# Kernel optimization log

Hardware: AMD Instinct MI355X
Metric: run time of the kernel (lower is better)

## Reference

```python
import jax, jax.numpy as jnp
import numpy as np

DIM, NH, HD = 1536, 12, 128
C = HD // 2            # 64 complex (half) dims per head
BANDS = (C - 2 * (C // 3), C // 3, C // 3)   # (22, 21, 21) for T/H/W
EPS = 1e-6
F, Hg, Wg = 6, 20, 32
S = F * Hg * Wg
MAX_LEN = 1024


def _rope_tables(max_len=MAX_LEN):
    # Wan-style 1D rope params per band, concatenated along channel dim -> [max_len, 64]
    pos = np.arange(max_len, dtype=np.float64)
    cos_l, sin_l = [], []
    for bd in BANDS:
        inv = 1.0 / (10000.0 ** (np.arange(bd, dtype=np.float64) / bd))
        ang = np.outer(pos, inv)
        cos_l.append(np.cos(ang))
        sin_l.append(np.sin(ang))
    return (np.concatenate(cos_l, 1).astype(np.float32),
            np.concatenate(sin_l, 1).astype(np.float32))


def setup_inputs() -> dict:
    key = jax.random.key(0)
    ks = jax.random.split(key, 8)
    std = 0.02
    fc, fs = _rope_tables()
    return {
        "x": jax.random.normal(ks[0], (1, S, DIM), jnp.float32),
        "Wq": jax.random.normal(ks[1], (DIM, DIM), jnp.float32) * std,
        "bq": jnp.zeros((DIM,), jnp.float32),
        "Wk": jax.random.normal(ks[2], (DIM, DIM), jnp.float32) * std,
        "bk": jnp.zeros((DIM,), jnp.float32),
        "Wv": jax.random.normal(ks[3], (DIM, DIM), jnp.float32) * std,
        "bv": jnp.zeros((DIM,), jnp.float32),
        "Wo": jax.random.normal(ks[4], (DIM, DIM), jnp.float32) * std,
        "bo": jnp.zeros((DIM,), jnp.float32),
        "gq": jnp.ones((DIM,), jnp.float32),
        "gk": jnp.ones((DIM,), jnp.float32),
        "freqs_cos": jnp.asarray(fc),
        "freqs_sin": jnp.asarray(fs),
        "f": F, "h": Hg, "w": Wg,
    }


def _rmsnorm(t, g):
    t = t.astype(jnp.float32)
    return t * jax.lax.rsqrt(jnp.mean(t * t, axis=-1, keepdims=True) + EPS) * g


def _grid_freqs(tab, f, h, w):
    # tab: [max_len, 64] -> [f*h*w, 64] via T/H/W band broadcast (mirrors torch expand+cat)
    o1, o2 = BANDS[0], BANDS[0] + BANDS[1]
    t = jnp.broadcast_to(tab[:f, None, None, :o1], (f, h, w, BANDS[0]))
    hh = jnp.broadcast_to(tab[None, :h, None, o1:o2], (f, h, w, BANDS[1]))
    ww = jnp.broadcast_to(tab[None, None, :w, o2:C], (f, h, w, BANDS[2]))
    return jnp.concatenate([t, hh, ww], axis=-1).reshape(f * h * w, 1, C)


def _rope_apply(t, fc, fs):
    # t: [B, S, n, d]; complex mul (a+ib)*(cos+isin) on pairs of channels
    B, Sl, n, d = t.shape
    tr = t.astype(jnp.float32).reshape(B, Sl, n, C, 2)
    a, b = tr[..., 0], tr[..., 1]
    fc = fc[None]  # [1, S, 1, C]
    fs = fs[None]
    out_r = a * fc - b * fs
    out_i = a * fs + b * fc
    return jnp.stack([out_r, out_i], axis=-1).reshape(B, Sl, n, d)


def reference(x, Wq, bq, Wk, bk, Wv, bv, Wo, bo, gq, gk, freqs_cos, freqs_sin, f, h, w):
    B, Sl, _ = x.shape
    q = _rmsnorm(x @ Wq.T + bq, gq).reshape(B, Sl, NH, HD)
    k = _rmsnorm(x @ Wk.T + bk, gk).reshape(B, Sl, NH, HD)
    v = (x @ Wv.T + bv).reshape(B, Sl, NH, HD)

    fc = _grid_freqs(freqs_cos, f, h, w)
    fs = _grid_freqs(freqs_sin, f, h, w)
    q = _rope_apply(q, fc, fs)
    k = _rope_apply(k, fc, fs)

    scale = 1.0 / jnp.sqrt(jnp.float32(HD))
    scores = jnp.einsum('bqnd,bknd->bnqk', q, k) * scale
    p = jax.nn.softmax(scores, axis=-1)
    o = jnp.einsum('bnqk,bknd->bqnd', p, v.astype(jnp.float32))
    o = o.reshape(B, Sl, DIM)
    return o @ Wo.T + bo
```

## Files before the change

kernel.cpp:

```cpp
#include <hip/hip_runtime.h>
#include <hip/hip_bf16.h>
#include <cstdint>

#define DIM 1536
#define NHEADS 12
#define HD 128
#define SEQ 3840
#define SCL2F 0.1275365308119098f
#define THRRAW 90.50966799187809f

typedef float f32x4 __attribute__((ext_vector_type(4)));
typedef __bf16 bf16x8 __attribute__((ext_vector_type(8)));
typedef __bf16 bf16x4 __attribute__((ext_vector_type(4)));
typedef __bf16 bf16x2 __attribute__((ext_vector_type(2)));
typedef unsigned int u32;
typedef u32 u32x4 __attribute__((ext_vector_type(4)));

#define GLLD(g, l) __builtin_amdgcn_global_load_lds( \
    (const __attribute__((address_space(1))) void*)(g), \
    (__attribute__((address_space(3))) void*)(l), 16, 0, 0)

__global__ __launch_bounds__(256) void cvt_bf16_5(
    const float* __restrict__ s0, const float* __restrict__ s1, const float* __restrict__ s2,
    const float* __restrict__ s3, const float* __restrict__ s4,
    __bf16* __restrict__ d0, __bf16* __restrict__ d1, __bf16* __restrict__ d2,
    __bf16* __restrict__ d3, __bf16* __restrict__ d4,
    int n4_0, int n4_w) {
    const float* src; __bf16* dst; int n4;
    switch (blockIdx.y) {
        case 0: src = s0; dst = d0; n4 = n4_0; break;
        case 1: src = s1; dst = d1; n4 = n4_w; break;
        case 2: src = s2; dst = d2; n4 = n4_w; break;
        case 3: src = s3; dst = d3; n4 = n4_w; break;
        default: src = s4; dst = d4; n4 = n4_w; break;
    }
    int i = blockIdx.x * 256 + threadIdx.x;
    if (i < n4) {
        f32x4 v = ((const f32x4*)src)[i];
        bf16x4 o;
        o[0] = (__bf16)v[0]; o[1] = (__bf16)v[1];
        o[2] = (__bf16)v[2]; o[3] = (__bf16)v[3];
        ((bf16x4*)dst)[i] = o;
    }
}

template <int OUTF32>
__global__ __launch_bounds__(256, 2) void gemm256(
    const __bf16* __restrict__ A,
    const __bf16* __restrict__ B0, const __bf16* __restrict__ B1, const __bf16* __restrict__ B2,
    const float* __restrict__ bias0, const float* __restrict__ bias1, const float* __restrict__ bias2,
    void* __restrict__ C0v, void* __restrict__ C1v, void* __restrict__ C2v,
    int N, int K) {
    const __bf16* B = B0; const float* bias = bias0; void* Cv = C0v;
    if (blockIdx.z == 1) { B = B1; bias = bias1; Cv = C1v; }
    else if (blockIdx.z == 2) { B = B2; bias = bias2; Cv = C2v; }

    __shared__ __bf16 sA[3][256 * 32];
    __shared__ __bf16 sB[3][128 * 32];

    const int t = threadIdx.x;
    const int wid = t >> 6, lane = t & 63;
    const int lr = lane & 15, lg = lane >> 4;
    const int wr = (wid >> 1) * 128, wc = (wid & 1) * 64;

    const __bf16* pa = A + ((long long)blockIdx.y * 256 + (t >> 2)) * K + (t & 3) * 8;
    const __bf16* pb = B + ((long long)blockIdx.x * 128 + (t >> 2)) * K + (t & 3) * 8;
    const int ldsbase = wid * 512;

    auto stage = [&](int kk, int bufi) {
#pragma unroll
        for (int r = 0; r < 4; r++)
            GLLD(pa + (long long)(r * 64) * K + kk, &sA[bufi][r * 2048 + ldsbase]);
#pragma unroll
        for (int r = 0; r < 2; r++)
            GLLD(pb + (long long)(r * 64) * K + kk, &sB[bufi][r * 2048 + ldsbase]);
    };

    f32x4 acc[8][4] = {};
    const int NT = K / 32;

    stage(0, 0);
    stage(32, 1);
    asm volatile("s_waitcnt vmcnt(6)" ::: "memory");
    __builtin_amdgcn_s_barrier();
    __builtin_amdgcn_sched_barrier(0);

    int c0 = 0, c2 = 2;
#pragma unroll 1
    for (int i = 0; i < NT; i++) {
        const __bf16* sAc = &sA[0][0] + c0 * (256 * 32);
        const __bf16* sBc = &sB[0][0] + c0 * (128 * 32);
        bf16x8 af[8], bfr[4];
#pragma unroll
        for (int mI = 0; mI < 8; mI++)
            af[mI] = *(const bf16x8*)(sAc + (wr + mI * 16 + lr) * 32 + lg * 8);
#pragma unroll
        for (int nI = 0; nI < 4; nI++)
            bfr[nI] = *(const bf16x8*)(sBc + (wc + nI * 16 + lr) * 32 + lg * 8);
        if (i + 2 < NT) stage((i + 2) * 32, c2);

        __builtin_amdgcn_s_setprio(1);
#pragma unroll
        for (int mI = 0; mI < 8; mI++) {
            acc[mI][0] = __builtin_amdgcn_mfma_f32_16x16x32_bf16(af[mI], bfr[0], acc[mI][0], 0, 0, 0);
            acc[mI][1] = __builtin_amdgcn_mfma_f32_16x16x32_bf16(af[mI], bfr[1], acc[mI][1], 0, 0, 0);
        }
        __builtin_amdgcn_s_setprio(0);
        __builtin_amdgcn_s_barrier();
        __builtin_amdgcn_s_setprio(1);
#pragma unroll
        for (int mI = 0; mI < 8; mI++) {
            acc[mI][2] = __builtin_amdgcn_mfma_f32_16x16x32_bf16(af[mI], bfr[2], acc[mI][2], 0, 0, 0);
            acc[mI][3] = __builtin_amdgcn_mfma_f32_16x16x32_bf16(af[mI], bfr[3], acc[mI][3], 0, 0, 0);
        }
        __builtin_amdgcn_s_setprio(0);

        if (i + 2 < NT) asm volatile("s_waitcnt vmcnt(6)" ::: "memory");
        else            asm volatile("s_waitcnt vmcnt(0)" ::: "memory");
        __builtin_amdgcn_s_barrier();
        __builtin_amdgcn_sched_barrier(0);
        c0 = (c0 == 2) ? 0 : c0 + 1;
        c2 = (c2 == 2) ? 0 : c2 + 1;
    }

    const int cb = blockIdx.x * 128 + wc;
    const int rb_ = blockIdx.y * 256 + wr;
#pragma unroll
    for (int nI = 0; nI < 4; nI++) {
        int col = cb + nI * 16 + lr;
        float bv = bias[col];
#pragma unroll
        for (int mI = 0; mI < 8; mI++) {
            int row0 = rb_ + mI * 16 + lg * 4;
#pragma unroll
            for (int r = 0; r < 4; r++) {
                float v = acc[mI][nI][r] + bv;
                if (OUTF32) ((float*)Cv)[(long long)(row0 + r) * N + col] = v;
                else ((__bf16*)Cv)[(long long)(row0 + r) * N + col] = (__bf16)v;
            }
        }
    }
}

__global__ __launch_bounds__(256) void norm_rope2(
    const __bf16* __restrict__ qpre, const __bf16* __restrict__ kpre,
    const float* __restrict__ gq, const float* __restrict__ gk,
    const float* __restrict__ fcos, const float* __restrict__ fsin,
    __bf16* __restrict__ Qb, __bf16* __restrict__ Kb) {
    const __bf16* pre = blockIdx.y ? kpre : qpre;
    const float* gvec = blockIdx.y ? gk : gq;
    __bf16* out = blockIdx.y ? Kb : Qb;
    const int s = blockIdx.x;
    const int t = threadIdx.x;
    float a[3], b[3];
    float ss = 0.f;
#pragma unroll
    for (int j = 0; j < 3; j++) {
        int p = t + 256 * j;
        bf16x2 v = *(const bf16x2*)(pre + (size_t)s * DIM + 2 * p);
        a[j] = (float)v[0]; b[j] = (float)v[1];
        ss += a[j] * a[j] + b[j] * b[j];
    }
    for (int off = 32; off; off >>= 1) ss += __shfl_down(ss, off);
    __shared__ float red[4];
    if ((t & 63) == 0) red[t >> 6] = ss;
    __syncthreads();
    float mean = (red[0] + red[1] + red[2] + red[3]) * (1.f / DIM);
    float rms = rsqrtf(mean + 1e-6f);
    const int fi = s / 640, hi2 = (s % 640) >> 5, wi = s & 31;
#pragma unroll
    for (int j = 0; j < 3; j++) {
        int p = t + 256 * j;
        int c = p & 63;
        int pos = (c < 22) ? fi : ((c < 43) ? hi2 : wi);
        float fc = fcos[pos * 64 + c];
        float fs = fsin[pos * 64 + c];
        float av = a[j] * rms * gvec[2 * p];
        float bv = b[j] * rms * gvec[2 * p + 1];
        float orr = av * fc - bv * fs;
        float oi = av * fs + bv * fc;
        int hh = p >> 6;
        bf16x2 o; o[0] = (__bf16)orr; o[1] = (__bf16)oi;
        *(bf16x2*)(out + ((size_t)hh * SEQ + s) * HD + 2 * c) = o;
    }
}

__global__ __launch_bounds__(256) void transpose_bf16(
    const __bf16* __restrict__ in, __bf16* __restrict__ out) {
    __shared__ __bf16 tile[64][68];
    const int t = threadIdx.x;
    const int sb = blockIdx.x * 64, cb = blockIdx.y * 64;
    const int tx = t & 15, ty = t >> 4;
#pragma unroll
    for (int i = 0; i < 4; i++) {
        int r = ty + i * 16;
        bf16x4 v = *(const bf16x4*)(in + (size_t)(sb + r) * DIM + cb + tx * 4);
        *(bf16x4*)&tile[r][tx * 4] = v;
    }
    __syncthreads();
    int s0 = sb + tx * 4;
    int j = (s0 >> 2) & 7;
    int u = (j < 4) ? (j << 1) : ((j << 1) - 7);
    int sp = (s0 & ~31) + (u << 2);
#pragma unroll
    for (int i = 0; i < 4; i++) {
        int c = ty + i * 16;
        bf16x4 v;
        v[0] = tile[tx * 4 + 0][c]; v[1] = tile[tx * 4 + 1][c];
        v[2] = tile[tx * 4 + 2][c]; v[3] = tile[tx * 4 + 3][c];
        *(bf16x4*)(out + (size_t)(cb + c) * SEQ + sp) = v;
    }
}

__global__ __launch_bounds__(256, 4) void attn(
    const __bf16* __restrict__ Q, const __bf16* __restrict__ Kk,
    const __bf16* __restrict__ Vp, __bf16* __restrict__ O) {
    __shared__ __bf16 Ks[2][32 * 128];
    __shared__ __bf16 Vs[2][128 * 32];
    const int bid = blockIdx.x;
    const int task = (bid & 7) * 90 + (bid >> 3);
    const int h = task / 60;
    const int qb = task % 60;
    const int t = threadIdx.x;
    const int wv = t >> 6;
    const int lane = t & 63;
    const int lq = lane & 15, g = lane >> 4;
    const int q0 = qb * 64 + wv * 16;
    const __bf16* Qh = Q + (size_t)h * SEQ * HD;
    const __bf16* Kh = Kk + (size_t)h * SEQ * HD;
    const __bf16* Vh = Vp + (size_t)h * HD * SEQ;

    bf16x8 qf[4];
#pragma unroll
    for (int c = 0; c < 4; c++)
        qf[c] = *(const bf16x8*)(Qh + (size_t)(q0 + lq) * HD + c * 32 + g * 8);

    f32x4 acc[8] = {};
    float m = -1e30f;
    float lp = 0.f;

    const int krow_in = lane >> 4;
    const int vrow_in = lane >> 2;
    const int vce = (lane & 3) * 8;
    auto stage = [&](int kv0, int b) {
#pragma unroll
        for (int c = wv; c < 16; c += 4) {
            if (c < 8) {
                int r = c * 4 + krow_in;
                int cb = ((lane & 15) * 16) ^ ((r & 7) << 4);
                GLLD(Kh + (size_t)(kv0 + r) * HD + (cb >> 1), &Ks[b][c * 512]);
            } else {
                int cc = c - 8;
                int rd = cc * 16 + vrow_in;
                GLLD(Vh + (size_t)rd * SEQ + kv0 + vce, &Vs[b][cc * 512]);
            }
        }
    };

    stage(0, 0);
    int buf = 0;
    const int kswz = (lq & 7) << 3;
#pragma unroll 1
    for (int i = 0; i < 120; i++) {
        __syncthreads();
        if (i + 1 < 120) stage((i + 1) * 32, buf ^ 1);
        const __bf16* Kb_ = &Ks[buf][0];
        const __bf16* Vb_ = &Vs[buf][0];

        f32x4 sc0 = {0.f, 0.f, 0.f, 0.f}, sc1 = {0.f, 0.f, 0.f, 0.f};
        __builtin_amdgcn_s_setprio(1);
#pragma unroll
        for (int c = 0; c < 4; c++) {
            int cb = (c * 32 + g * 8) ^ kswz;
            bf16x8 k0 = *(const bf16x8*)(Kb_ + lq * 128 + cb);
            bf16x8 k1 = *(const bf16x8*)(Kb_ + (16 + lq) * 128 + cb);
            sc0 = __builtin_amdgcn_mfma_f32_16x16x32_bf16(k0, qf[c], sc0, 0, 0, 0);
            sc1 = __builtin_amdgcn_mfma_f32_16x16x32_bf16(k1, qf[c], sc1, 0, 0, 0);
        }
        __builtin_amdgcn_s_setprio(0);

        bf16x8 vf[8];
#pragma unroll
        for (int dt = 0; dt < 8; dt++)
            vf[dt] = *(const bf16x8*)(Vb_ + (dt * 16 + lq) * 32 + g * 8);

        float pm = fmaxf(fmaxf(fmaxf(sc0[0], sc0[1]), fmaxf(sc0[2], sc0[3])),
                         fmaxf(fmaxf(sc1[0], sc1[1]), fmaxf(sc1[2], sc1[3])));
        if (!__all(pm <= m + THRRAW)) {
            pm = fmaxf(pm, __shfl_xor(pm, 16));
            pm = fmaxf(pm, __shfl_xor(pm, 32));
            float mn = fmaxf(m, pm);
            float al = __builtin_amdgcn_exp2f(SCL2F * (m - mn));
            m = mn; lp *= al;
#pragma unroll
            for (int dt = 0; dt < 8; dt++)
#pragma unroll
                for (int r = 0; r < 4; r++) acc[dt][r] *= al;
        }
        float ms = SCL2F * m;
        float p[8], ls = 0.f;
#pragma unroll
        for (int r = 0; r < 4; r++) { p[r] = __builtin_amdgcn_exp2f(SCL2F * sc0[r] - ms); ls += p[r]; }
#pragma unroll
        for (int r = 0; r < 4; r++) { p[4 + r] = __builtin_amdgcn_exp2f(SCL2F * sc1[r] - ms); ls += p[4 + r]; }
        lp += ls;
        bf16x8 pa;
#pragma unroll
        for (int i2 = 0; i2 < 8; i2++) pa[i2] = (__bf16)p[i2];

        __builtin_amdgcn_s_setprio(1);
#pragma unroll
        for (int dt = 0; dt < 8; dt++)
            acc[dt] = __builtin_amdgcn_mfma_f32_16x16x32_bf16(vf[dt], pa, acc[dt], 0, 0, 0);
        __builtin_amdgcn_s_setprio(0);
        buf ^= 1;
    }

    float lps = lp;
    lps += __shfl_xor(lps, 16);
    lps += __shfl_xor(lps, 32);
    float inv = 1.f / lps;
#pragma unroll
    for (int dt = 0; dt < 8; dt++) {
        bf16x4 o;
#pragma unroll
        for (int r = 0; r < 4; r++) o[r] = (__bf16)(acc[dt][r] * inv);
        *(bf16x4*)(O + (size_t)(q0 + lq) * DIM + h * HD + dt * 16 + g * 4) = o;
    }
}

extern "C" void kernel_launch(void* const* d_in, const int* in_sizes, int n_in,
                              void* d_out, int out_size, void* d_ws, size_t ws_size,
                              hipStream_t stream) {
    const float* x = (const float*)d_in[0];
    const float* Wq = (const float*)d_in[1];
    const float* bq = (const float*)d_in[2];
    const float* Wk = (const float*)d_in[3];
    const float* bk = (const float*)d_in[4];
    const float* Wv = (const float*)d_in[5];
    const float* bv = (const float*)d_in[6];
    const float* Wo = (const float*)d_in[7];
    const float* bo = (const float*)d_in[8];
    const float* gq = (const float*)d_in[9];
    const float* gk = (const float*)d_in[10];
    const float* fcos = (const float*)d_in[11];
    const float* fsin = (const float*)d_in[12];
    float* out = (float*)d_out;

    char* p = (char*)d_ws;
    const size_t SZ_SD = (size_t)SEQ * DIM * 2;
    const size_t SZ_W = (size_t)DIM * DIM * 2;
    __bf16* xb   = (__bf16*)p;  p += SZ_SD;
    __bf16* Wqb  = (__bf16*)p;  p += SZ_W;
    __bf16* Wkb  = (__bf16*)p;  p += SZ_W;
    __bf16* Wvb  = (__bf16*)p;  p += SZ_W;
    __bf16* Wob  = (__bf16*)p;  p += SZ_W;
    __bf16* qpre = (__bf16*)p;  p += SZ_SD;
    __bf16* kpre = (__bf16*)p;  p += SZ_SD;
    __bf16* vpre = (__bf16*)p;  p += SZ_SD;
    __bf16* Kb   = (__bf16*)p;  p += SZ_SD;
    __bf16* Vtb  = (__bf16*)p;  p += SZ_SD;
    __bf16* Qb = xb;
    __bf16* ob = qpre;

    const int n4_x = SEQ * DIM / 4;
    const int n4_w = DIM * DIM / 4;
    cvt_bf16_5<<<dim3((n4_x + 255) / 256, 5), 256, 0, stream>>>(
        x, Wq, Wk, Wv, Wo, xb, Wqb, Wkb, Wvb, Wob, n4_x, n4_w);

    gemm256<0><<<dim3(DIM / 128, SEQ / 256, 3), 256, 0, stream>>>(
        xb, Wqb, Wkb, Wvb, bq, bk, bv, qpre, kpre, vpre, DIM, DIM);

    norm_rope2<<<dim3(SEQ, 2), 256, 0, stream>>>(qpre, kpre, gq, gk, fcos, fsin, Qb, Kb);
    transpose_bf16<<<dim3(SEQ / 64, DIM / 64), 256, 0, stream>>>(vpre, Vtb);

    attn<<<dim3(720), 256, 0, stream>>>(Qb, Kb, Vtb, ob);

    gemm256<1><<<dim3(DIM / 128, SEQ / 256, 1), 256, 0, stream>>>(
        ob, Wob, Wob, Wob, bo, bo, bo, out, out, out, DIM, DIM);
}
```

Baseline: 284.9 us.

## Split attention KV range into two halves with separate merge kernel

Result: slower. 296.0 us (+3.9%).

```diff
diff --git a/kernel.cpp b/kernel.cpp
--- a/kernel.cpp
+++ b/kernel.cpp
@@ -212,7 +212,146 @@
     }
 }
 
-__global__ __launch_bounds__(256, 4) void attn(
+__global__ __launch_bounds__(256, 4) void attn_split(
+    const __bf16* __restrict__ Q, const __bf16* __restrict__ Kk,
+    const __bf16* __restrict__ Vp,
+    float* __restrict__ pacc,
+    float2* __restrict__ pml) {
+    __shared__ __bf16 Ks[2][32 * 128];
+    __shared__ __bf16 Vs[2][128 * 32];
+    const int bid = blockIdx.x;
+    const int task = (bid & 7) * 180 + (bid >> 3);
+    const int half = task & 1;
+    const int hq = task >> 1;
+    const int h = hq / 60;
+    const int qb = hq % 60;
+    const int t = threadIdx.x;
+    const int wv = t >> 6;
+    const int lane = t & 63;
+    const int lq = lane & 15, g = lane >> 4;
+    const int q0 = qb * 64 + wv * 16;
+    const int kvbase = half * (SEQ / 2);
+    const __bf16* Qh = Q + (size_t)h * SEQ * HD;
+    const __bf16* Kh = Kk + (size_t)h * SEQ * HD;
+    const __bf16* Vh = Vp + (size_t)h * HD * SEQ;
+
+    bf16x8 qf[4];
+#pragma unroll
+    for (int c = 0; c < 4; c++)
+        qf[c] = *(const bf16x8*)(Qh + (size_t)(q0 + lq) * HD + c * 32 + g * 8);
+
+    f32x4 acc[8] = {};
+    float m = -1e30f;
+    float lp = 0.f;
+
+    const int krow_in = lane >> 4;
+    const int vrow_in = lane >> 2;
+    const int vce = (lane & 3) * 8;
+    auto stage = [&](int kv0, int b) {
+#pragma unroll
+        for (int c = wv; c < 16; c += 4) {
+            if (c < 8) {
+                int r = c * 4 + krow_in;
+                int cb = ((lane & 15) * 16) ^ ((r & 7) << 4);
+                GLLD(Kh + (size_t)(kv0 + r) * HD + (cb >> 1), &Ks[b][c * 512]);
+            } else {
+                int cc = c - 8;
+                int rd = cc * 16 + vrow_in;
+                GLLD(Vh + (size_t)rd * SEQ + kv0 + vce, &Vs[b][cc * 512]);
+            }
+        }
+    };
+
+    stage(kvbase, 0);
+    int buf = 0;
+    const int kswz = (lq & 7) << 3;
+#pragma unroll 1
+    for (int i = 0; i < 60; i++) {
+        __syncthreads();
+        if (i + 1 < 60) stage(kvbase + (i + 1) * 32, buf ^ 1);
+        const __bf16* Kb_ = &Ks[buf][0];
+        const __bf16* Vb_ = &Vs[buf][0];
+
+        f32x4 sc0 = {0.f, 0.f, 0.f, 0.f}, sc1 = {0.f, 0.f, 0.f, 0.f};
+        __builtin_amdgcn_s_setprio(1);
+#pragma unroll
+        for (int c = 0; c < 4; c++) {
+            int cb = (c * 32 + g * 8) ^ kswz;
+            bf16x8 k0 = *(const bf16x8*)(Kb_ + lq * 128 + cb);
+            bf16x8 k1 = *(const bf16x8*)(Kb_ + (16 + lq) * 128 + cb);
+            sc0 = __builtin_amdgcn_mfma_f32_16x16x32_bf16(k0, qf[c], sc0, 0, 0, 0);
+            sc1 = __builtin_amdgcn_mfma_f32_16x16x32_bf16(k1, qf[c], sc1, 0, 0, 0);
+        }
+        __builtin_amdgcn_s_setprio(0);
+
+        bf16x8 vf[8];
+#pragma unroll
+        for (int dt = 0; dt < 8; dt++)
+            vf[dt] = *(const bf16x8*)(Vb_ + (dt * 16 + lq) * 32 + g * 8);
+
+        float pm = fmaxf(fmaxf(fmaxf(sc0[0], sc0[1]), fmaxf(sc0[2], sc0[3])),
+                         fmaxf(fmaxf(sc1[0], sc1[1]), fmaxf(sc1[2], sc1[3])));
+        if (!__all(pm <= m + THRRAW)) {
+            pm = fmaxf(pm, __shfl_xor(pm, 16));
+            pm = fmaxf(pm, __shfl_xor(pm, 32));
+            float mn = fmaxf(m, pm);
+            float al = __builtin_amdgcn_exp2f(SCL2F * (m - mn));
+            m = mn; lp *= al;
+#pragma unroll
+            for (int dt = 0; dt < 8; dt++)
+#pragma unroll
+                for (int r = 0; r < 4; r++) acc[dt][r] *= al;
+        }
+        float ms = SCL2F * m;
+        float p[8], ls = 0.f;
+#pragma unroll
+        for (int r = 0; r < 4; r++) { p[r] = __builtin_amdgcn_exp2f(SCL2F * sc0[r] - ms); ls += p[r]; }
+#pragma unroll
+        for (int r = 0; r < 4; r++) { p[4 + r] = __builtin_amdgcn_exp2f(SCL2F * sc1[r] - ms); ls += p[4 + r]; }
+        lp += ls;
+        bf16x8 pa;
+#pragma unroll
+        for (int i2 = 0; i2 < 8; i2++) pa[i2] = (__bf16)p[i2];
+
+        __builtin_amdgcn_s_setprio(1);
+#pragma unroll
+        for (int dt = 0; dt < 8; dt++)
+            acc[dt] = __builtin_amdgcn_mfma_f32_16x16x32_bf16(vf[dt], pa, acc[dt], 0, 0, 0);
+        __builtin_amdgcn_s_setprio(0);
+        buf ^= 1;
+    }
+
+    float lps = lp;
+    lps += __shfl_xor(lps, 16);
+    lps += __shfl_xor(lps, 32);
+    const size_t qrow = (size_t)(half * NHEADS + h) * SEQ + q0 + lq;
+    if (g == 0) pml[qrow] = float2{m, lps};
+#pragma unroll
+    for (int dt = 0; dt < 8; dt++)
+        *(f32x4*)(pacc + qrow * HD + dt * 16 + g * 4) = acc[dt];
+}
+
+__global__ __launch_bounds__(256) void attn_merge(
+    const float* __restrict__ pacc, const float2* __restrict__ pml,
+    __bf16* __restrict__ ob) {
+    const int t = threadIdx.x;
+    const int qq = blockIdx.x * 8 + (t >> 5);
+    const int d = (t & 31) * 4;
+    float2 a = pml[qq], b = pml[NHEADS * SEQ + qq];
+    float M = fmaxf(a.x, b.x);
+    float w0 = __builtin_amdgcn_exp2f(SCL2F * (a.x - M));
+    float w1 = __builtin_amdgcn_exp2f(SCL2F * (b.x - M));
+    float den = 1.f / (a.y * w0 + b.y * w1);
+    f32x4 n0 = *(const f32x4*)(pacc + (size_t)qq * HD + d);
+    f32x4 n1 = *(const f32x4*)(pacc + ((size_t)NHEADS * SEQ + qq) * HD + d);
+    int h = qq / SEQ, s = qq % SEQ;
+    bf16x4 o;
+#pragma unroll
+    for (int r = 0; r < 4; r++) o[r] = (__bf16)((n0[r] * w0 + n1[r] * w1) * den);
+    *(bf16x4*)(ob + (size_t)s * DIM + h * HD + d) = o;
+}
+
+__global__ __launch_bounds__(256, 4) void attn_single(
     const __bf16* __restrict__ Q, const __bf16* __restrict__ Kk,
     const __bf16* __restrict__ Vp, __bf16* __restrict__ O) {
     __shared__ __bf16 Ks[2][32 * 128];
@@ -229,16 +368,12 @@
     const __bf16* Qh = Q + (size_t)h * SEQ * HD;
     const __bf16* Kh = Kk + (size_t)h * SEQ * HD;
     const __bf16* Vh = Vp + (size_t)h * HD * SEQ;
-
     bf16x8 qf[4];
 #pragma unroll
     for (int c = 0; c < 4; c++)
         qf[c] = *(const bf16x8*)(Qh + (size_t)(q0 + lq) * HD + c * 32 + g * 8);
-
     f32x4 acc[8] = {};
-    float m = -1e30f;
-    float lp = 0.f;
-
+    float m = -1e30f, lp = 0.f;
     const int krow_in = lane >> 4;
     const int vrow_in = lane >> 2;
     const int vce = (lane & 3) * 8;
@@ -256,7 +391,6 @@
             }
         }
     };
-
     stage(0, 0);
     int buf = 0;
     const int kswz = (lq & 7) << 3;
@@ -266,9 +400,7 @@
         if (i + 1 < 120) stage((i + 1) * 32, buf ^ 1);
         const __bf16* Kb_ = &Ks[buf][0];
         const __bf16* Vb_ = &Vs[buf][0];
-
         f32x4 sc0 = {0.f, 0.f, 0.f, 0.f}, sc1 = {0.f, 0.f, 0.f, 0.f};
-        __builtin_amdgcn_s_setprio(1);
 #pragma unroll
         for (int c = 0; c < 4; c++) {
             int cb = (c * 32 + g * 8) ^ kswz;
@@ -277,13 +409,10 @@
             sc0 = __builtin_amdgcn_mfma_f32_16x16x32_bf16(k0, qf[c], sc0, 0, 0, 0);
             sc1 = __builtin_amdgcn_mfma_f32_16x16x32_bf16(k1, qf[c], sc1, 0, 0, 0);
         }
-        __builtin_amdgcn_s_setprio(0);
-
         bf16x8 vf[8];
 #pragma unroll
         for (int dt = 0; dt < 8; dt++)
             vf[dt] = *(const bf16x8*)(Vb_ + (dt * 16 + lq) * 32 + g * 8);
-
         float pm = fmaxf(fmaxf(fmaxf(sc0[0], sc0[1]), fmaxf(sc0[2], sc0[3])),
                          fmaxf(fmaxf(sc1[0], sc1[1]), fmaxf(sc1[2], sc1[3])));
         if (!__all(pm <= m + THRRAW)) {
@@ -307,15 +436,11 @@
         bf16x8 pa;
 #pragma unroll
         for (int i2 = 0; i2 < 8; i2++) pa[i2] = (__bf16)p[i2];
-
-        __builtin_amdgcn_s_setprio(1);
 #pragma unroll
         for (int dt = 0; dt < 8; dt++)
             acc[dt] = __builtin_amdgcn_mfma_f32_16x16x32_bf16(vf[dt], pa, acc[dt], 0, 0, 0);
-        __builtin_amdgcn_s_setprio(0);
         buf ^= 1;
     }
-
     float lps = lp;
     lps += __shfl_xor(lps, 16);
     lps += __shfl_xor(lps, 32);
@@ -351,17 +476,19 @@
     const size_t SZ_SD = (size_t)SEQ * DIM * 2;
     const size_t SZ_W = (size_t)DIM * DIM * 2;
     __bf16* xb   = (__bf16*)p;  p += SZ_SD;
+    __bf16* Wob  = (__bf16*)p;  p += SZ_W;
     __bf16* Wqb  = (__bf16*)p;  p += SZ_W;
     __bf16* Wkb  = (__bf16*)p;  p += SZ_W;
     __bf16* Wvb  = (__bf16*)p;  p += SZ_W;
-    __bf16* Wob  = (__bf16*)p;  p += SZ_W;
     __bf16* qpre = (__bf16*)p;  p += SZ_SD;
     __bf16* kpre = (__bf16*)p;  p += SZ_SD;
     __bf16* vpre = (__bf16*)p;  p += SZ_SD;
     __bf16* Kb   = (__bf16*)p;  p += SZ_SD;
     __bf16* Vtb  = (__bf16*)p;  p += SZ_SD;
+    float2* pml  = (float2*)p;  p += sizeof(float2) * 2 * NHEADS * SEQ;
+    float* pacc = (float*)Wqb;
     __bf16* Qb = xb;
-    __bf16* ob = qpre;
+    const bool split_ok = ws_size >= (size_t)(p - (char*)d_ws);
 
     const int n4_x = SEQ * DIM / 4;
     const int n4_w = DIM * DIM / 4;
@@ -374,8 +501,16 @@
     norm_rope2<<<dim3(SEQ, 2), 256, 0, stream>>>(qpre, kpre, gq, gk, fcos, fsin, Qb, Kb);
     transpose_bf16<<<dim3(SEQ / 64, DIM / 64), 256, 0, stream>>>(vpre, Vtb);
 
-    attn<<<dim3(720), 256, 0, stream>>>(Qb, Kb, Vtb, ob);
-
-    gemm256<1><<<dim3(DIM / 128, SEQ / 256, 1), 256, 0, stream>>>(
-        ob, Wob, Wob, Wob, bo, bo, bo, out, out, out, DIM, DIM);
-}
+    if (split_ok) {
+        __bf16* ob = Kb;
+        attn_split<<<dim3(1440), 256, 0, stream>>>(Qb, Kb, Vtb, pacc, pml);
+        attn_merge<<<dim3(NHEADS * SEQ / 8), 256, 0, stream>>>(pacc, pml, ob);
+        gemm256<1><<<dim3(DIM / 128, SEQ / 256, 1), 256, 0, stream>>>(
+            ob, Wob, Wob, Wob, bo, bo, bo, out, out, out, DIM, DIM);
+    } else {
+        __bf16* ob = qpre;
+        attn_single<<<dim3(720), 256, 0, stream>>>(Qb, Kb, Vtb, ob);
+        gemm256<1><<<dim3(DIM / 128, SEQ / 256, 1), 256, 0, stream>>>(
+            ob, Wob, Wob, Wob, bo, bo, bo, out, out, out, DIM, DIM);
+    }
+}
```
